# Kernel optimization log

Hardware: AMD Instinct MI355X
Metric: run time of the kernel (lower is better)

The kernel has to match this reference:

```python
import jax, jax.numpy as jnp
import numpy as np

R = 3          # bilateral radius -> 7x7 window (kernel_size=7, dilation=1)
NIC = 12       # num_input_channels per frame
NHS = 1        # num_hidden_states
DN = ('NCHW', 'OIHW', 'NCHW')


def _conv(x, w, b, groups=1):
    y = jax.lax.conv_general_dilated(x, w, (1, 1), 'SAME',
                                     dimension_numbers=DN,
                                     feature_group_count=groups)
    return y + b[None, :, None, None]


def _lcn(x, k=3):
    # run_lcn(color, 3): local contrast normalization with k x k box window, per channel
    C = x.shape[1]
    box = jnp.ones((C, 1, k, k), x.dtype) / (k * k)
    zb = jnp.zeros((C,), x.dtype)
    mean = _conv(x, box, zb, groups=C)
    mean2 = _conv(x * x, box, zb, groups=C)
    var = jnp.maximum(mean2 - mean * mean, 0.0)
    return (x - mean) * jax.lax.rsqrt(var + 1e-5)


def _bilateral(dyn, feat, scale):
    # cross-bilateral: weights from guide features, applied to dynamic channels
    B, _, H, W = dyn.shape
    pad = ((0, 0), (0, 0), (R, R), (R, R))
    fp = jnp.pad(feat, pad, mode='edge')
    dp = jnp.pad(dyn, pad, mode='edge')
    s = scale[None, :, None, None]            # [1,8,1,1] per-feature inverse sigma^2
    acc = jnp.zeros_like(dyn)
    wsum = jnp.zeros((B, 1, H, W), dyn.dtype)
    for dy in range(2 * R + 1):
        for dx in range(2 * R + 1):
            fq = fp[:, :, dy:dy + H, dx:dx + W]
            w = jnp.exp(-jnp.sum(s * (feat - fq) ** 2, axis=1, keepdims=True))
            acc = acc + w * dp[:, :, dy:dy + H, dx:dx + W]
            wsum = wsum + w
    return acc / (wsum + 1e-8)


def _forward(x, alpha, cr_w0, cr_b0, cr_w1, cr_b1, cr_w2, cr_b2,
             hs_w0, hs_b0, hs_w1, hs_b1, hs_w2, hs_b2,
             filt_w, filt_b, filt_scale):
    B, CT, H, W = x.shape
    num_frames = CT // NIC
    a = alpha[0]
    temporal = jnp.zeros((B, 3 + NHS, H, W), x.dtype)
    outs = []
    for i in range(num_frames):
        frame = x[:, i * NIC:(i + 1) * NIC]
        color, albedo, fixed = frame[:, :3], frame[:, 3:6], frame[:, 3:]
        rec_in = jnp.concatenate([_lcn(color), color], axis=1)           # 6ch
        h = jax.nn.relu(_conv(rec_in, cr_w0, cr_b0))
        h = jax.nn.relu(_conv(h, cr_w1, cr_b1))
        recombined = _conv(h, cr_w2, cr_b2)                              # 3ch
        hs_in = jnp.concatenate([recombined, fixed], axis=1)             # 12ch
        h = jax.nn.relu(_conv(hs_in, hs_w0, hs_b0))
        h = jax.nn.relu(_conv(h, hs_w1, hs_b1))
        hidden = _conv(h, hs_w2, hs_b2)                                  # 1ch
        dynamic = jnp.concatenate([color, hidden], axis=1)               # 4ch
        if i != 0:
            dynamic = a * dynamic + (1.0 - a) * temporal
        filtered = jnp.concatenate([dynamic, fixed], axis=1)             # 13ch
        for k in range(5):
            feat = _conv(filtered, filt_w[k], filt_b[k])                 # 8 guide features
            fdyn = _bilateral(filtered[:, :3 + NHS], feat, filt_scale[k])
            filtered = jnp.concatenate([fdyn, fixed], axis=1)
        outs.append(albedo * filtered[:, :3])
        temporal = filtered[:, :3 + NHS]
    return jnp.concatenate(outs, axis=1)   # [B, 3*num_frames, H, W]


def setup_inputs():
    key = jax.random.key(0)
    ks = jax.random.split(key, 12)
    w = lambda k, s: (0.1 * jax.random.normal(k, s)).astype(jnp.float32)
    z = lambda s: jnp.zeros(s, jnp.float32)
    return {
        'x': jax.random.normal(ks[0], (1, 48, 720, 1280), dtype=jnp.float32),
        'alpha': jnp.full((1,), 0.5, jnp.float32),
        'cr_w0': w(ks[1], (6, 6, 3, 3)),   'cr_b0': z((6,)),
        'cr_w1': w(ks[2], (12, 6, 3, 3)),  'cr_b1': z((12,)),
        'cr_w2': w(ks[3], (3, 12, 3, 3)),  'cr_b2': z((3,)),
        'hs_w0': w(ks[4], (12, 12, 3, 3)), 'hs_b0': z((12,)),
        'hs_w1': w(ks[5], (12, 12, 3, 3)), 'hs_b1': z((12,)),
        'hs_w2': w(ks[6], (1, 12, 3, 3)),  'hs_b2': z((1,)),
        'filt_w': w(ks[7], (5, 8, 13, 3, 3)), 'filt_b': z((5, 8)),
        'filt_scale': 0.5 * jax.random.uniform(ks[8], (5, 8), dtype=jnp.float32),
    }


def reference(x, alpha, cr_w0, cr_b0, cr_w1, cr_b1, cr_w2, cr_b2,
              hs_w0, hs_b0, hs_w1, hs_b1, hs_w2, hs_b2,
              filt_w, filt_b, filt_scale):
    return _forward(x, alpha, cr_w0, cr_b0, cr_w1, cr_b1, cr_w2, cr_b2,
                    hs_w0, hs_b0, hs_w1, hs_b1, hs_w2, hs_b2,
                    filt_w, filt_b, filt_scale)
```

## Files before the change

kernel.cpp:

```cpp
#include <hip/hip_runtime.h>

#define HH 720
#define WW 1280
#define HWP (HH*WW)

static constexpr int NFRM = 4;
typedef _Float16 h2 __attribute__((ext_vector_type(2)));

template <int PX, int C0, int C1, int COUT, bool RELU>
__global__ __launch_bounds__(128) void conv3x3_v3(const float* __restrict__ in0, long i0fs,
                                                  const float* __restrict__ in1, long i1fs,
                                                  const float* __restrict__ w,
                                                  const float* __restrict__ b,
                                                  float* __restrict__ out, long ofs) {
  constexpr int CIN = C0 + C1;
  constexpr int NBX = WW / (16 * PX);
  int fi = blockIdx.y;
  in0 += (size_t)fi * i0fs;
  out += (size_t)fi * ofs;
  const float* in1f = nullptr;
  if constexpr (C1 > 0) in1f = in1 + (size_t)fi * i1fs;

  int bx = blockIdx.x % NBX;
  int by = blockIdx.x / NBX;
  int tx = threadIdx.x & 15;
  int ty = threadIdx.x >> 4;
  int gx0 = bx * (16 * PX) + tx * PX;
  int gy  = by * 8 + ty;

  float acc[COUT][PX];
  #pragma unroll
  for (int co = 0; co < COUT; ++co) {
    float bv = b[co];
    #pragma unroll
    for (int px = 0; px < PX; ++px) acc[co][px] = bv;
  }

  const bool lok = (gx0 > 0);
  const bool rok = (gx0 + PX < WW);

  for (int c = 0; c < CIN; ++c) {
    const float* ch;
    if constexpr (C1 > 0)
      ch = (c < C0) ? (in0 + (size_t)c * HWP) : (in1f + (size_t)(c - C0) * HWP);
    else
      ch = in0 + (size_t)c * HWP;
    float r[3][PX + 2];
    #pragma unroll
    for (int ky = 0; ky < 3; ++ky) {
      int iy = gy + ky - 1;
      bool yok = (iy >= 0) && (iy < HH);
      const float* row = ch + (ptrdiff_t)iy * WW;
      #pragma unroll
      for (int j = 0; j < PX / 4; ++j) {
        float4 a = yok ? *reinterpret_cast<const float4*>(row + gx0 + 4 * j)
                       : make_float4(0.f, 0.f, 0.f, 0.f);
        r[ky][1 + 4*j + 0] = a.x; r[ky][1 + 4*j + 1] = a.y;
        r[ky][1 + 4*j + 2] = a.z; r[ky][1 + 4*j + 3] = a.w;
      }
      r[ky][0]      = (yok && lok) ? row[gx0 - 1]  : 0.f;
      r[ky][PX + 1] = (yok && rok) ? row[gx0 + PX] : 0.f;
    }
    #pragma unroll
    for (int co = 0; co < COUT; ++co) {
      #pragma unroll
      for (int ky = 0; ky < 3; ++ky) {
        #pragma unroll
        for (int kx = 0; kx < 3; ++kx) {
          float wv = w[((co * CIN + c) * 3 + ky) * 3 + kx];
          #pragma unroll
          for (int px = 0; px < PX; ++px)
            acc[co][px] = fmaf(wv, r[ky][px + kx], acc[co][px]);
        }
      }
    }
  }

  size_t p = (size_t)gy * WW + gx0;
  #pragma unroll
  for (int co = 0; co < COUT; ++co) {
    #pragma unroll
    for (int j = 0; j < PX / 4; ++j) {
      float4 o;
      o.x = RELU ? fmaxf(acc[co][4*j+0], 0.f) : acc[co][4*j+0];
      o.y = RELU ? fmaxf(acc[co][4*j+1], 0.f) : acc[co][4*j+1];
      o.z = RELU ? fmaxf(acc[co][4*j+2], 0.f) : acc[co][4*j+2];
      o.w = RELU ? fmaxf(acc[co][4*j+3], 0.f) : acc[co][4*j+3];
      *reinterpret_cast<float4*>(out + (size_t)co * HWP + p + 4*j) = o;
    }
  }
}

__global__ __launch_bounds__(128) void lcn_v3(const float* __restrict__ x, long ifs,
                                              float* __restrict__ out, long ofs) {
  constexpr int NBX = WW / 128;
  int fi = blockIdx.y;
  const float* color = x + (size_t)fi * ifs;
  out += (size_t)fi * ofs;
  int bx = blockIdx.x % NBX;
  int by = blockIdx.x / NBX;
  int tx = threadIdx.x & 15;
  int ty = threadIdx.x >> 4;
  int gx0 = bx * 128 + tx * 8;
  int gy  = by * 8 + ty;
  const bool lok = (gx0 > 0);
  const bool rok = (gx0 + 8 < WW);
  size_t p = (size_t)gy * WW + gx0;

  #pragma unroll
  for (int c = 0; c < 3; ++c) {
    const float* ch = color + (size_t)c * HWP;
    float r[3][10];
    #pragma unroll
    for (int ky = 0; ky < 3; ++ky) {
      int iy = gy + ky - 1;
      bool yok = (iy >= 0) && (iy < HH);
      const float* row = ch + (ptrdiff_t)iy * WW;
      float4 a = yok ? *reinterpret_cast<const float4*>(row + gx0)
                     : make_float4(0.f, 0.f, 0.f, 0.f);
      float4 q = yok ? *reinterpret_cast<const float4*>(row + gx0 + 4)
                     : make_float4(0.f, 0.f, 0.f, 0.f);
      r[ky][0] = (yok && lok) ? row[gx0 - 1] : 0.f;
      r[ky][1] = a.x; r[ky][2] = a.y; r[ky][3] = a.z; r[ky][4] = a.w;
      r[ky][5] = q.x; r[ky][6] = q.y; r[ky][7] = q.z; r[ky][8] = q.w;
      r[ky][9] = (yok && rok) ? row[gx0 + 8] : 0.f;
    }
    float lcnv[8], cv[8];
    #pragma unroll
    for (int px = 0; px < 8; ++px) {
      float s = 0.f, s2 = 0.f;
      #pragma unroll
      for (int ky = 0; ky < 3; ++ky)
        #pragma unroll
        for (int kx = 0; kx < 3; ++kx) {
          float v = r[ky][px + kx];
          s += v; s2 = fmaf(v, v, s2);
        }
      float mean = s * (1.f / 9.f);
      float mean2 = s2 * (1.f / 9.f);
      float var = fmaxf(mean2 - mean * mean, 0.f);
      cv[px] = r[1][px + 1];
      lcnv[px] = (cv[px] - mean) * rsqrtf(var + 1e-5f);
    }
    #pragma unroll
    for (int h = 0; h < 2; ++h) {
      float4 o0 = make_float4(lcnv[4*h+0], lcnv[4*h+1], lcnv[4*h+2], lcnv[4*h+3]);
      float4 o1 = make_float4(cv[4*h+0], cv[4*h+1], cv[4*h+2], cv[4*h+3]);
      *reinterpret_cast<float4*>(out + (size_t)c * HWP + p + 4*h) = o0;
      *reinterpret_cast<float4*>(out + (size_t)(3 + c) * HWP + p + 4*h) = o1;
    }
  }
}

__global__ __launch_bounds__(256) void blend_v3(const float* __restrict__ color,
                                                const float* __restrict__ hid,
                                                const float* __restrict__ temporal,
                                                const float* __restrict__ alpha,
                                                float* __restrict__ dyn, int first) {
  int i = (blockIdx.x * 256 + threadIdx.x) * 4;
  if (i >= HWP) return;
  if (first) {
    #pragma unroll
    for (int c = 0; c < 3; ++c)
      *reinterpret_cast<float4*>(dyn + (size_t)c * HWP + i) =
          *reinterpret_cast<const float4*>(color + (size_t)c * HWP + i);
    *reinterpret_cast<float4*>(dyn + 3 * (size_t)HWP + i) =
        *reinterpret_cast<const float4*>(hid + i);
  } else {
    float a = alpha[0];
    float om = 1.f - a;
    #pragma unroll
    for (int c = 0; c < 4; ++c) {
      const float* src = (c < 3) ? (color + (size_t)c * HWP) : hid;
      float4 cv = *reinterpret_cast<const float4*>(src + i);
      float4 tv = *reinterpret_cast<const float4*>(temporal + (size_t)c * HWP + i);
      float4 o;
      o.x = a * cv.x + om * tv.x;
      o.y = a * cv.y + om * tv.y;
      o.z = a * cv.z + om * tv.z;
      o.w = a * cv.w + om * tv.w;
      *reinterpret_cast<float4*>(dyn + (size_t)c * HWP + i) = o;
    }
  }
}

#define BC 38
#define BR 22
#define BNPX (BC*BR)
#define BPAD 840

__device__ __forceinline__ int bswz(int lin) { return lin ^ ((lin >> 3) & 7); }

template <bool OUT>
__global__ __launch_bounds__(256, 4) void bilateral_v5(const float* __restrict__ dyn,
                                                       const float* __restrict__ feat,
                                                       const float* __restrict__ scale,
                                                       float* __restrict__ outdyn,
                                                       const float* __restrict__ albedo,
                                                       float* __restrict__ outp) {
  __shared__ uint4  ft[BPAD];
  __shared__ float4 dt[BPAD];
  int bx = blockIdx.x % 40;
  int by = blockIdx.x / 40;
  int tid = threadIdx.x;

  for (int i = tid; i < BNPX; i += 256) {
    int py = i / BC;
    int px = i - py * BC;
    int gy = min(max(by * 16 + py - 3, 0), HH - 1);
    int gx = min(max(bx * 32 + px - 3, 0), WW - 1);
    size_t g = (size_t)gy * WW + gx;
    int w = bswz(i);
    dt[w] = make_float4(dyn[g], dyn[HWP + g], dyn[2*(size_t)HWP + g], dyn[3*(size_t)HWP + g]);
    uint4 u;
    u.x = __builtin_bit_cast(unsigned, __builtin_amdgcn_cvt_pkrtz(feat[g],                 feat[HWP + g]));
    u.y = __builtin_bit_cast(unsigned, __builtin_amdgcn_cvt_pkrtz(feat[2*(size_t)HWP + g], feat[3*(size_t)HWP + g]));
    u.z = __builtin_bit_cast(unsigned, __builtin_amdgcn_cvt_pkrtz(feat[4*(size_t)HWP + g], feat[5*(size_t)HWP + g]));
    u.w = __builtin_bit_cast(unsigned, __builtin_amdgcn_cvt_pkrtz(feat[6*(size_t)HWP + g], feat[7*(size_t)HWP + g]));
    ft[w] = u;
  }
  __syncthreads();

  int txg = tid & 15;
  int ty  = tid >> 4;

  float sv[8];
  #pragma unroll
  for (int c = 0; c < 8; ++c) sv[c] = scale[c];

  float sfc[2][8], A[2];
  #pragma unroll
  for (int p = 0; p < 2; ++p) {
    int lin = (ty + 3) * BC + txg * 2 + 3 + p;
    uint4 u = ft[bswz(lin)];
    h2 a0 = __builtin_bit_cast(h2, u.x), a1 = __builtin_bit_cast(h2, u.y);
    h2 a2 = __builtin_bit_cast(h2, u.z), a3 = __builtin_bit_cast(h2, u.w);
    float fc[8] = {(float)a0[0], (float)a0[1], (float)a1[0], (float)a1[1],
                   (float)a2[0], (float)a2[1], (float)a3[0], (float)a3[1]};
    float aa = 0.f;
    #pragma unroll
    for (int c = 0; c < 8; ++c) {
      sfc[p][c] = sv[c] * fc[c];
      aa = fmaf(sfc[p][c], fc[c], aa);
    }
    A[p] = aa;
  }

  float acc[2][4], ws2[2];
  #pragma unroll
  for (int p = 0; p < 2; ++p) {
    ws2[p] = 0.f;
    acc[p][0] = acc[p][1] = acc[p][2] = acc[p][3] = 0.f;
  }

  for (int dy = 0; dy < 7; ++dy) {
    int rowb = (ty + dy) * BC + txg * 2;
    #pragma unroll
    for (int dx = 0; dx < 8; ++dx) {
      int w = bswz(rowb + dx);
      float4 dv = dt[w];
      uint4 u = ft[w];
      h2 a0 = __builtin_bit_cast(h2, u.x), a1 = __builtin_bit_cast(h2, u.y);
      h2 a2 = __builtin_bit_cast(h2, u.z), a3 = __builtin_bit_cast(h2, u.w);
      float f[8] = {(float)a0[0], (float)a0[1], (float)a1[0], (float)a1[1],
                    (float)a2[0], (float)a2[1], (float)a3[0], (float)a3[1]};
      float B = 0.f;
      #pragma unroll
      for (int c = 0; c < 8; ++c) B = fmaf(sv[c] * f[c], f[c], B);
      #pragma unroll
      for (int p = 0; p < 2; ++p) {
        if (dx - p >= 0 && dx - p <= 6) {
          float C = 0.f;
          #pragma unroll
          for (int c = 0; c < 8; ++c) C = fmaf(sfc[p][c], f[c], C);
          float e = fmaf(-2.f, C, A[p] + B);
          float wgt = __expf(-e);
          acc[p][0] = fmaf(wgt, dv.x, acc[p][0]);
          acc[p][1] = fmaf(wgt, dv.y, acc[p][1]);
          acc[p][2] = fmaf(wgt, dv.z, acc[p][2]);
          acc[p][3] = fmaf(wgt, dv.w, acc[p][3]);
          ws2[p] += wgt;
        }
      }
    }
  }

  int gy = by * 16 + ty;
  int gx0 = bx * 32 + txg * 2;
  size_t p0 = (size_t)gy * WW + gx0;
  float inv0 = 1.f / (ws2[0] + 1e-8f);
  float inv1 = 1.f / (ws2[1] + 1e-8f);
  #pragma unroll
  for (int c = 0; c < 4; ++c) {
    float2 o = make_float2(acc[0][c] * inv0, acc[1][c] * inv1);
    *reinterpret_cast<float2*>(outdyn + (size_t)c * HWP + p0) = o;
    if (OUT && c < 3) {
      float2 al = *reinterpret_cast<const float2*>(albedo + (size_t)c * HWP + p0);
      float2 oo = make_float2(o.x * al.x, o.y * al.y);
      *reinterpret_cast<float2*>(outp + (size_t)c * HWP + p0) = oo;
    }
  }
}

extern "C" void kernel_launch(void* const* d_in, const int* in_sizes, int n_in,
                              void* d_out, int out_size, void* d_ws, size_t ws_size,
                              hipStream_t stream) {
  const float* x          = (const float*)d_in[0];
  const float* alpha      = (const float*)d_in[1];
  const float* cr_w0      = (const float*)d_in[2];
  const float* cr_b0      = (const float*)d_in[3];
  const float* cr_w1      = (const float*)d_in[4];
  const float* cr_b1      = (const float*)d_in[5];
  const float* cr_w2      = (const float*)d_in[6];
  const float* cr_b2      = (const float*)d_in[7];
  const float* hs_w0      = (const float*)d_in[8];
  const float* hs_b0      = (const float*)d_in[9];
  const float* hs_w1      = (const float*)d_in[10];
  const float* hs_b1      = (const float*)d_in[11];
  const float* hs_w2      = (const float*)d_in[12];
  const float* hs_b2      = (const float*)d_in[13];
  const float* filt_w     = (const float*)d_in[14];
  const float* filt_b     = (const float*)d_in[15];
  const float* filt_scale = (const float*)d_in[16];

  float* out = (float*)d_out;
  float* ws  = (float*)d_ws;
  const size_t P = (size_t)HWP;

  bool batched = ws_size >= (size_t)108 * P * sizeof(float);
  float *bufA, *bufB, *dynT, *dynA, *dynB, *hid, *feat;
  if (batched) {
    bufA = ws;            bufB = ws + 48 * P;
    dynT = ws + 96 * P;   dynA = ws + 100 * P;  dynB = ws + 104 * P;
  } else {
    bufA = ws;            bufB = ws + 12 * P;
    dynT = ws + 24 * P;   dynA = ws + 28 * P;   dynB = ws + 32 * P;
  }
  hid  = bufA;
  feat = bufB;

  const int NB8 = (WW / 128) * (HH / 8);
  const int NB4 = (WW / 64)  * (HH / 8);
  const int NBE = HWP / (256 * 4);
  const int NBB = (WW / 32)  * (HH / 16);

  if (batched) {
    dim3 g(NB8, NFRM);
    lcn_v3<<<g, 128, 0, stream>>>(x, 12 * P, bufA, 6 * P);
    conv3x3_v3<8, 6, 0, 6,  true ><<<g, 128, 0, stream>>>(bufA, 6 * P,  nullptr, 0, cr_w0, cr_b0, bufB, 6 * P);
    conv3x3_v3<8, 6, 0, 12, true ><<<g, 128, 0, stream>>>(bufB, 6 * P,  nullptr, 0, cr_w1, cr_b1, bufA, 12 * P);
    conv3x3_v3<8, 12, 0, 3, false><<<g, 128, 0, stream>>>(bufA, 12 * P, nullptr, 0, cr_w2, cr_b2, bufB, 3 * P);
    conv3x3_v3<8, 3, 9, 12, true ><<<g, 128, 0, stream>>>(bufB, 3 * P,  x + 3 * P, 12 * P, hs_w0, hs_b0, bufA, 12 * P);
    conv3x3_v3<8, 12, 0, 12, true><<<g, 128, 0, stream>>>(bufA, 12 * P, nullptr, 0, hs_w1, hs_b1, bufB, 12 * P);
    conv3x3_v3<8, 12, 0, 1, false><<<g, 128, 0, stream>>>(bufB, 12 * P, nullptr, 0, hs_w2, hs_b2, hid, P);
  }

  for (int f = 0; f < NFRM; ++f) {
    const float* frame = x + (size_t)f * 12 * P;
    const float* fixedp = frame + 3 * P;

    if (!batched) {
      dim3 g(NB8, 1);
      lcn_v3<<<g, 128, 0, stream>>>(frame, 0, bufA, 0);
      conv3x3_v3<8, 6, 0, 6,  true ><<<g, 128, 0, stream>>>(bufA, 0, nullptr, 0, cr_w0, cr_b0, bufB, 0);
      conv3x3_v3<8, 6, 0, 12, true ><<<g, 128, 0, stream>>>(bufB, 0, nullptr, 0, cr_w1, cr_b1, bufA, 0);
      conv3x3_v3<8, 12, 0, 3, false><<<g, 128, 0, stream>>>(bufA, 0, nullptr, 0, cr_w2, cr_b2, bufB, 0);
      conv3x3_v3<8, 3, 9, 12, true ><<<g, 128, 0, stream>>>(bufB, 0, fixedp, 0, hs_w0, hs_b0, bufA, 0);
      conv3x3_v3<8, 12, 0, 12, true><<<g, 128, 0, stream>>>(bufA, 0, nullptr, 0, hs_w1, hs_b1, bufB, 0);
      conv3x3_v3<8, 12, 0, 1, false><<<g, 128, 0, stream>>>(bufB, 0, nullptr, 0, hs_w2, hs_b2, hid, 0);
    }

    const float* hidf = batched ? (hid + (size_t)f * P) : hid;
    blend_v3<<<NBE, 256, 0, stream>>>(frame, hidf, dynT, alpha, dynA, f == 0 ? 1 : 0);

    float* cur = dynA;
    float* nxt = dynB;
    for (int k = 0; k < 5; ++k) {
      conv3x3_v3<4, 4, 9, 8, false><<<dim3(NB4, 1), 128, 0, stream>>>(
          cur, 0, fixedp, 0, filt_w + (size_t)k * 8 * 13 * 9, filt_b + k * 8, feat, 0);
      if (k < 4) {
        bilateral_v5<false><<<NBB, 256, 0, stream>>>(cur, feat, filt_scale + k * 8, nxt,
                                                     nullptr, nullptr);
        float* t = cur; cur = nxt; nxt = t;
      } else {
        bilateral_v5<true><<<NBB, 256, 0, stream>>>(cur, feat, filt_scale + k * 8, dynT,
                                                    fixedp, out + (size_t)f * 3 * P);
      }
    }
  }
}
```

Before: 2.630 ms.

## Fuse filter-guide 3x3 conv into bilateral kernel with fp16 shared-memory halo

The per-iteration 8-channel guide conv now runs inside the bilateral kernel. It loads a 13-channel fp16 halo tile into shared memory, computes the features for the 38x22 window (recomputing the halo) and writes them straight to LDS, so the feature map no longer makes a global round trip. The dynamic channels are also read from the staged fp16 input, which reduces their precision. Separately, the recurrent and hidden-state convs switch from 8 to 4 pixels per thread. The fused kernel costs extra conv work on halos, larger LDS use and lower occupancy.

New measurement: 3.335 ms. +26.8%, slower.

```diff
diff --git a/kernel.cpp b/kernel.cpp
--- a/kernel.cpp
+++ b/kernel.cpp
@@ -6,6 +6,7 @@
 
 static constexpr int NFRM = 4;
 typedef _Float16 h2 __attribute__((ext_vector_type(2)));
+typedef _Float16 h4 __attribute__((ext_vector_type(4)));
 
 template <int PX, int C0, int C1, int COUT, bool RELU>
 __global__ __launch_bounds__(128) void conv3x3_v3(const float* __restrict__ in0, long i0fs,
@@ -184,40 +185,134 @@
   }
 }
 
-#define BC 38
-#define BR 22
-#define BNPX (BC*BR)
-#define BPAD 840
+#define FBC 38
+#define FBR 22
+#define FBPAD 840
+#define INW 40
+#define INH 24
+#define INPLANE (INW*INH)
 
 __device__ __forceinline__ int bswz(int lin) { return lin ^ ((lin >> 3) & 7); }
+__device__ __forceinline__ unsigned pkh(float a, float b) {
+  return __builtin_bit_cast(unsigned, __builtin_amdgcn_cvt_pkrtz(a, b));
+}
 
 template <bool OUT>
-__global__ __launch_bounds__(256, 4) void bilateral_v5(const float* __restrict__ dyn,
-                                                       const float* __restrict__ feat,
-                                                       const float* __restrict__ scale,
-                                                       float* __restrict__ outdyn,
-                                                       const float* __restrict__ albedo,
-                                                       float* __restrict__ outp) {
-  __shared__ uint4  ft[BPAD];
-  __shared__ float4 dt[BPAD];
-  int bx = blockIdx.x % 40;
-  int by = blockIdx.x / 40;
-  int tid = threadIdx.x;
-
-  for (int i = tid; i < BNPX; i += 256) {
-    int py = i / BC;
-    int px = i - py * BC;
-    int gy = min(max(by * 16 + py - 3, 0), HH - 1);
-    int gx = min(max(bx * 32 + px - 3, 0), WW - 1);
-    size_t g = (size_t)gy * WW + gx;
-    int w = bswz(i);
-    dt[w] = make_float4(dyn[g], dyn[HWP + g], dyn[2*(size_t)HWP + g], dyn[3*(size_t)HWP + g]);
-    uint4 u;
-    u.x = __builtin_bit_cast(unsigned, __builtin_amdgcn_cvt_pkrtz(feat[g],                 feat[HWP + g]));
-    u.y = __builtin_bit_cast(unsigned, __builtin_amdgcn_cvt_pkrtz(feat[2*(size_t)HWP + g], feat[3*(size_t)HWP + g]));
-    u.z = __builtin_bit_cast(unsigned, __builtin_amdgcn_cvt_pkrtz(feat[4*(size_t)HWP + g], feat[5*(size_t)HWP + g]));
-    u.w = __builtin_bit_cast(unsigned, __builtin_amdgcn_cvt_pkrtz(feat[6*(size_t)HWP + g], feat[7*(size_t)HWP + g]));
-    ft[w] = u;
+__global__ __launch_bounds__(256, 3) void filt_fused(
+    const float* __restrict__ cur,
+    const float* __restrict__ fixedp,
+    const float* __restrict__ wconv,
+    const float* __restrict__ bias,
+    const float* __restrict__ scale,
+    float* __restrict__ outdyn,
+    const float* __restrict__ albedo,
+    float* __restrict__ outp)
+{
+  __shared__ _Float16 pin[13 * INPLANE + 8];
+  __shared__ uint4  ft[FBPAD];
+  __shared__ float4 dt[FBPAD];
+  const int bx = blockIdx.x % 40;
+  const int by = blockIdx.x / 40;
+  const int X0 = bx * 32, Y0 = by * 16;
+  const int tid = threadIdx.x;
+
+  for (int i = tid; i < 13 * INH * (INW / 2); i += 256) {
+    int c   = i / (INH * (INW / 2));
+    int rem = i - c * (INH * (INW / 2));
+    int iy  = rem / (INW / 2);
+    int ix  = (rem - iy * (INW / 2)) * 2;
+    int gy = Y0 - 4 + iy;
+    int gx = X0 - 4 + ix;
+    const float* src = (c < 4) ? (cur + (size_t)c * HWP) : (fixedp + (size_t)(c - 4) * HWP);
+    float v0 = 0.f, v1 = 0.f;
+    if (gy >= 0 && gy < HH) {
+      const float* row = src + (size_t)gy * WW;
+      if (gx >= 0 && gx + 1 < WW) {
+        float2 t = *reinterpret_cast<const float2*>(row + gx);
+        v0 = t.x; v1 = t.y;
+      } else {
+        if (gx >= 0 && gx < WW) v0 = row[gx];
+        if (gx + 1 >= 0 && gx + 1 < WW) v1 = row[gx + 1];
+      }
+    }
+    h2 hv; hv[0] = (_Float16)v0; hv[1] = (_Float16)v1;
+    *reinterpret_cast<h2*>(&pin[c * INPLANE + iy * INW + ix]) = hv;
+  }
+  __syncthreads();
+
+  const bool interior = (bx > 0) && (bx < 39) && (by > 0) && (by < 44);
+  const int xlo = 0 - (X0 - 3), xhi = (WW - 1) - (X0 - 3);
+  const int ylo = 0 - (Y0 - 3), yhi = (HH - 1) - (Y0 - 3);
+  {
+    int ctx = tid % 10, cty = tid / 10;
+    if (cty < FBR) {
+      int fx0 = ctx * 4;
+      float acc[8][4];
+      #pragma unroll
+      for (int co = 0; co < 8; ++co) {
+        float bv = bias[co];
+        acc[co][0] = bv; acc[co][1] = bv; acc[co][2] = bv; acc[co][3] = bv;
+      }
+      int fyc = min(max(cty, ylo), yhi);
+      if (interior) {
+        for (int ci = 0; ci < 13; ++ci) {
+          #pragma unroll
+          for (int ky = 0; ky < 3; ++ky) {
+            const _Float16* rp = &pin[ci * INPLANE + (cty + ky) * INW + fx0];
+            h4 a = *reinterpret_cast<const h4*>(rp);
+            h4 b = *reinterpret_cast<const h4*>(rp + 4);
+            float rr[6] = {(float)a[0], (float)a[1], (float)a[2], (float)a[3],
+                           (float)b[0], (float)b[1]};
+            #pragma unroll
+            for (int co = 0; co < 8; ++co) {
+              const float* wp = &wconv[((co * 13 + ci) * 3 + ky) * 3];
+              float w0 = wp[0], w1 = wp[1], w2 = wp[2];
+              #pragma unroll
+              for (int px = 0; px < 4; ++px)
+                acc[co][px] = fmaf(w0, rr[px], fmaf(w1, rr[px + 1], fmaf(w2, rr[px + 2], acc[co][px])));
+            }
+          }
+        }
+      } else {
+        for (int ci = 0; ci < 13; ++ci) {
+          #pragma unroll
+          for (int ky = 0; ky < 3; ++ky) {
+            const _Float16* rp = &pin[ci * INPLANE + (fyc + ky) * INW];
+            #pragma unroll
+            for (int px = 0; px < 4; ++px) {
+              int fxc = min(max(fx0 + px, xlo), xhi);
+              float r0 = (float)rp[fxc], r1 = (float)rp[fxc + 1], r2 = (float)rp[fxc + 2];
+              #pragma unroll
+              for (int co = 0; co < 8; ++co) {
+                const float* wp = &wconv[((co * 13 + ci) * 3 + ky) * 3];
+                acc[co][px] = fmaf(wp[0], r0, fmaf(wp[1], r1, fmaf(wp[2], r2, acc[co][px])));
+              }
+            }
+          }
+        }
+      }
+      #pragma unroll
+      for (int px = 0; px < 4; ++px) {
+        int fx = fx0 + px;
+        if (fx < FBC) {
+          int wsl = bswz(cty * FBC + fx);
+          uint4 u;
+          u.x = pkh(acc[0][px], acc[1][px]);
+          u.y = pkh(acc[2][px], acc[3][px]);
+          u.z = pkh(acc[4][px], acc[5][px]);
+          u.w = pkh(acc[6][px], acc[7][px]);
+          ft[wsl] = u;
+          int fxc = min(max(fx, xlo), xhi);
+          int ii = (fyc + 1) * INW + (fxc + 1);
+          float4 d;
+          d.x = (float)pin[0 * INPLANE + ii];
+          d.y = (float)pin[1 * INPLANE + ii];
+          d.z = (float)pin[2 * INPLANE + ii];
+          d.w = (float)pin[3 * INPLANE + ii];
+          dt[wsl] = d;
+        }
+      }
+    }
   }
   __syncthreads();
 
@@ -231,7 +326,7 @@
   float sfc[2][8], A[2];
   #pragma unroll
   for (int p = 0; p < 2; ++p) {
-    int lin = (ty + 3) * BC + txg * 2 + 3 + p;
+    int lin = (ty + 3) * FBC + txg * 2 + 3 + p;
     uint4 u = ft[bswz(lin)];
     h2 a0 = __builtin_bit_cast(h2, u.x), a1 = __builtin_bit_cast(h2, u.y);
     h2 a2 = __builtin_bit_cast(h2, u.z), a3 = __builtin_bit_cast(h2, u.w);
@@ -254,7 +349,7 @@
   }
 
   for (int dy = 0; dy < 7; ++dy) {
-    int rowb = (ty + dy) * BC + txg * 2;
+    int rowb = (ty + dy) * FBC + txg * 2;
     #pragma unroll
     for (int dx = 0; dx < 8; ++dx) {
       int w = bswz(rowb + dx);
@@ -285,8 +380,8 @@
     }
   }
 
-  int gy = by * 16 + ty;
-  int gx0 = bx * 32 + txg * 2;
+  int gy = Y0 + ty;
+  int gx0 = X0 + txg * 2;
   size_t p0 = (size_t)gy * WW + gx0;
   float inv0 = 1.f / (ws2[0] + 1e-8f);
   float inv1 = 1.f / (ws2[1] + 1e-8f);
@@ -328,7 +423,7 @@
   const size_t P = (size_t)HWP;
 
   bool batched = ws_size >= (size_t)108 * P * sizeof(float);
-  float *bufA, *bufB, *dynT, *dynA, *dynB, *hid, *feat;
+  float *bufA, *bufB, *dynT, *dynA, *dynB, *hid;
   if (batched) {
     bufA = ws;            bufB = ws + 48 * P;
     dynT = ws + 96 * P;   dynA = ws + 100 * P;  dynB = ws + 104 * P;
@@ -336,38 +431,37 @@
     bufA = ws;            bufB = ws + 12 * P;
     dynT = ws + 24 * P;   dynA = ws + 28 * P;   dynB = ws + 32 * P;
   }
-  hid  = bufA;
-  feat = bufB;
+  hid = bufA;
 
   const int NB8 = (WW / 128) * (HH / 8);
   const int NB4 = (WW / 64)  * (HH / 8);
   const int NBE = HWP / (256 * 4);
-  const int NBB = (WW / 32)  * (HH / 16);
+  const int NBF = (WW / 32)  * (HH / 16);
 
   if (batched) {
-    dim3 g(NB8, NFRM);
-    lcn_v3<<<g, 128, 0, stream>>>(x, 12 * P, bufA, 6 * P);
-    conv3x3_v3<8, 6, 0, 6,  true ><<<g, 128, 0, stream>>>(bufA, 6 * P,  nullptr, 0, cr_w0, cr_b0, bufB, 6 * P);
-    conv3x3_v3<8, 6, 0, 12, true ><<<g, 128, 0, stream>>>(bufB, 6 * P,  nullptr, 0, cr_w1, cr_b1, bufA, 12 * P);
-    conv3x3_v3<8, 12, 0, 3, false><<<g, 128, 0, stream>>>(bufA, 12 * P, nullptr, 0, cr_w2, cr_b2, bufB, 3 * P);
-    conv3x3_v3<8, 3, 9, 12, true ><<<g, 128, 0, stream>>>(bufB, 3 * P,  x + 3 * P, 12 * P, hs_w0, hs_b0, bufA, 12 * P);
-    conv3x3_v3<8, 12, 0, 12, true><<<g, 128, 0, stream>>>(bufA, 12 * P, nullptr, 0, hs_w1, hs_b1, bufB, 12 * P);
-    conv3x3_v3<8, 12, 0, 1, false><<<g, 128, 0, stream>>>(bufB, 12 * P, nullptr, 0, hs_w2, hs_b2, hid, P);
+    dim3 g8(NB8, NFRM), g4(NB4, NFRM);
+    lcn_v3<<<g8, 128, 0, stream>>>(x, 12 * P, bufA, 6 * P);
+    conv3x3_v3<4, 6, 0, 6,  true ><<<g4, 128, 0, stream>>>(bufA, 6 * P,  nullptr, 0, cr_w0, cr_b0, bufB, 6 * P);
+    conv3x3_v3<4, 6, 0, 12, true ><<<g4, 128, 0, stream>>>(bufB, 6 * P,  nullptr, 0, cr_w1, cr_b1, bufA, 12 * P);
+    conv3x3_v3<4, 12, 0, 3, false><<<g4, 128, 0, stream>>>(bufA, 12 * P, nullptr, 0, cr_w2, cr_b2, bufB, 3 * P);
+    conv3x3_v3<4, 3, 9, 12, true ><<<g4, 128, 0, stream>>>(bufB, 3 * P,  x + 3 * P, 12 * P, hs_w0, hs_b0, bufA, 12 * P);
+    conv3x3_v3<4, 12, 0, 12, true><<<g4, 128, 0, stream>>>(bufA, 12 * P, nullptr, 0, hs_w1, hs_b1, bufB, 12 * P);
+    conv3x3_v3<4, 12, 0, 1, false><<<g4, 128, 0, stream>>>(bufB, 12 * P, nullptr, 0, hs_w2, hs_b2, hid, P);
   }
 
   for (int f = 0; f < NFRM; ++f) {
-    const float* frame = x + (size_t)f * 12 * P;
+    const float* frame  = x + (size_t)f * 12 * P;
     const float* fixedp = frame + 3 * P;
 
     if (!batched) {
-      dim3 g(NB8, 1);
-      lcn_v3<<<g, 128, 0, stream>>>(frame, 0, bufA, 0);
-      conv3x3_v3<8, 6, 0, 6,  true ><<<g, 128, 0, stream>>>(bufA, 0, nullptr, 0, cr_w0, cr_b0, bufB, 0);
-      conv3x3_v3<8, 6, 0, 12, true ><<<g, 128, 0, stream>>>(bufB, 0, nullptr, 0, cr_w1, cr_b1, bufA, 0);
-      conv3x3_v3<8, 12, 0, 3, false><<<g, 128, 0, stream>>>(bufA, 0, nullptr, 0, cr_w2, cr_b2, bufB, 0);
-      conv3x3_v3<8, 3, 9, 12, true ><<<g, 128, 0, stream>>>(bufB, 0, fixedp, 0, hs_w0, hs_b0, bufA, 0);
-      conv3x3_v3<8, 12, 0, 12, true><<<g, 128, 0, stream>>>(bufA, 0, nullptr, 0, hs_w1, hs_b1, bufB, 0);
-      conv3x3_v3<8, 12, 0, 1, false><<<g, 128, 0, stream>>>(bufB, 0, nullptr, 0, hs_w2, hs_b2, hid, 0);
+      dim3 g8(NB8, 1), g4(NB4, 1);
+      lcn_v3<<<g8, 128, 0, stream>>>(frame, 0, bufA, 0);
+      conv3x3_v3<4, 6, 0, 6,  true ><<<g4, 128, 0, stream>>>(bufA, 0, nullptr, 0, cr_w0, cr_b0, bufB, 0);
+      conv3x3_v3<4, 6, 0, 12, true ><<<g4, 128, 0, stream>>>(bufB, 0, nullptr, 0, cr_w1, cr_b1, bufA, 0);
+      conv3x3_v3<4, 12, 0, 3, false><<<g4, 128, 0, stream>>>(bufA, 0, nullptr, 0, cr_w2, cr_b2, bufB, 0);
+      conv3x3_v3<4, 3, 9, 12, true ><<<g4, 128, 0, stream>>>(bufB, 0, fixedp, 0, hs_w0, hs_b0, bufA, 0);
+      conv3x3_v3<4, 12, 0, 12, true><<<g4, 128, 0, stream>>>(bufA, 0, nullptr, 0, hs_w1, hs_b1, bufB, 0);
+      conv3x3_v3<4, 12, 0, 1, false><<<g4, 128, 0, stream>>>(bufB, 0, nullptr, 0, hs_w2, hs_b2, hid, 0);
     }
 
     const float* hidf = batched ? (hid + (size_t)f * P) : hid;
@@ -376,16 +470,17 @@
     float* cur = dynA;
     float* nxt = dynB;
     for (int k = 0; k < 5; ++k) {
-      conv3x3_v3<4, 4, 9, 8, false><<<dim3(NB4, 1), 128, 0, stream>>>(
-          cur, 0, fixedp, 0, filt_w + (size_t)k * 8 * 13 * 9, filt_b + k * 8, feat, 0);
+      const float* wk = filt_w + (size_t)k * 8 * 13 * 9;
+      const float* bk = filt_b + k * 8;
+      const float* sk = filt_scale + k * 8;
       if (k < 4) {
-        bilateral_v5<false><<<NBB, 256, 0, stream>>>(cur, feat, filt_scale + k * 8, nxt,
-                                                     nullptr, nullptr);
+        filt_fused<false><<<NBF, 256, 0, stream>>>(cur, fixedp, wk, bk, sk, nxt,
+                                                   nullptr, nullptr);
         float* t = cur; cur = nxt; nxt = t;
       } else {
-        bilateral_v5<true><<<NBB, 256, 0, stream>>>(cur, feat, filt_scale + k * 8, dynT,
-                                                    fixedp, out + (size_t)f * 3 * P);
-      }
-    }
-  }
-}
+        filt_fused<true><<<NBF, 256, 0, stream>>>(cur, fixedp, wk, bk, sk, dynT,
+                                                  fixedp, out + (size_t)f * 3 * P);
+      }
+    }
+  }
+}
```
